# Kernel tuning notes

Hardware: AMD Instinct MI355X
Metric: run time of the kernel (lower is better)

Reference implementation:

```python
import jax, jax.numpy as jnp
import numpy as np

B, S, D, H = 4, 2048, 1024, 16
HD = D // H  # head_dim = 64


def setup_inputs() -> dict:
    key = jax.random.key(0)
    ks = jax.random.split(key, 10)
    sc = 0.02
    return {
        "data": jax.random.normal(ks[0], (B, S, D), jnp.float32),
        "context": jax.random.normal(ks[1], (B, S, D), jnp.float32),
        "Wq": jax.random.normal(ks[2], (D, D), jnp.float32) * sc,
        "bq": jnp.zeros((D,), jnp.float32),
        "Wk": jax.random.normal(ks[3], (D, D), jnp.float32) * sc,
        "bk": jnp.zeros((D,), jnp.float32),
        "Wv": jax.random.normal(ks[4], (D, D), jnp.float32) * sc,
        "bv": jnp.zeros((D,), jnp.float32),
        "Wo": jax.random.normal(ks[5], (D, D), jnp.float32) * sc,
        "bo": jnp.zeros((D,), jnp.float32),
    }


def reference(data, context, Wq, bq, Wk, bk, Wv, bv, Wo, bo):
    # Q/K/V projections (nn.Linear: x @ W^T + b; here weights stored as [in, out])
    Q = data @ Wq + bq            # [B,S,D]
    K = context @ Wk + bk
    V = context @ Wv + bv
    # split heads -> [B,H,S,HD]
    Q = Q.reshape(B, S, H, HD).transpose(0, 2, 1, 3)
    K = K.reshape(B, S, H, HD).transpose(0, 2, 1, 3)
    V = V.reshape(B, S, H, HD).transpose(0, 2, 1, 3)
    scale = jnp.sqrt(jnp.asarray(HD, Q.dtype))
    Z = jnp.einsum("bhqd,bhkd->bhqk", Q, K) / scale   # [B,H,S,S]
    # causal mask: row >= col allowed
    row = jnp.arange(S)[:, None]
    col = jnp.arange(S)[None, :]
    Z = jnp.where(row >= col, Z, jnp.asarray(-jnp.inf, Z.dtype))
    Z = jax.nn.softmax(Z, axis=-1)
    out = jnp.einsum("bhqk,bhkd->bhqd", Z, V)         # [B,H,S,HD]
    out = out.transpose(0, 2, 1, 3).reshape(B, S, D)
    return out @ Wo + bo
```

## Files before the change

### kernel.cpp

```cpp
#include <hip/hip_runtime.h>
#include <hip/hip_bf16.h>

#define B_ 4
#define S_ 2048
#define D_ 1024
#define H_ 16
#define HD_ 64
#define M_ (B_*S_)

typedef __bf16 bf16;
typedef __bf16 bf16v4 __attribute__((ext_vector_type(4)));
typedef __bf16 bf16v8 __attribute__((ext_vector_type(8)));
typedef float f32x4 __attribute__((ext_vector_type(4)));
typedef float f32x16 __attribute__((ext_vector_type(16)));

#define GLDS(gp, lp) __builtin_amdgcn_global_load_lds( \
    (const __attribute__((address_space(1))) void*)(gp), \
    (__attribute__((address_space(3))) void*)(lp), 16, 0, 0)

__global__ void cast_bf16_kernel(const float* __restrict__ in, bf16* __restrict__ out, int n) {
    int i = (blockIdx.x * blockDim.x + threadIdx.x) * 8;
    if (i >= n) return;
    const float4* p = reinterpret_cast<const float4*>(in + i);
    float4 a = p[0], b = p[1];
    bf16v8 o;
    o[0] = (bf16)a.x; o[1] = (bf16)a.y; o[2] = (bf16)a.z; o[3] = (bf16)a.w;
    o[4] = (bf16)b.x; o[5] = (bf16)b.y; o[6] = (bf16)b.z; o[7] = (bf16)b.w;
    *reinterpret_cast<bf16v8*>(out + i) = o;
}

__global__ void transpose_cast_kernel(const float* __restrict__ W, bf16* __restrict__ Wt,
                                      int K, int N, float scale) {
    __shared__ float tile[32][33];
    int kb = blockIdx.y * 32, nb = blockIdx.x * 32;
    int t = threadIdx.x;
    int c = t & 31, r0 = t >> 5;
    for (int i = 0; i < 4; ++i) {
        int r = r0 + i * 8;
        tile[r][c] = W[(size_t)(kb + r) * N + nb + c];
    }
    __syncthreads();
    for (int i = 0; i < 4; ++i) {
        int r = r0 + i * 8;
        Wt[(size_t)(nb + r) * K + kb + c] = (bf16)(tile[c][r] * scale);
    }
}

__global__ void transpose_v_kernel(const bf16* __restrict__ Vb, bf16* __restrict__ Vt) {
    __shared__ bf16 tile[32][33];
    int sb = blockIdx.x * 32;
    int z = blockIdx.y;
    int dt = z & 1, bh = z >> 1;
    int b = bh >> 4, h = bh & 15;
    int t = threadIdx.x;
    int c = t & 31, r0 = t >> 5;
    for (int i = 0; i < 4; ++i) {
        int r = r0 + i * 8;
        tile[r][c] = Vb[(size_t)(b * S_ + sb + r) * D_ + h * HD_ + dt * 32 + c];
    }
    __syncthreads();
    for (int i = 0; i < 4; ++i) {
        int r = r0 + i * 8;
        Vt[((size_t)bh * HD_ + dt * 32 + r) * S_ + sb + c] = tile[c][r];
    }
}

template<bool OUT_F32>
__global__ __launch_bounds__(256) void gemm128_kernel(const bf16* __restrict__ A,
                                                      const bf16* __restrict__ Bt,
                                                      const float* __restrict__ bias,
                                                      float bias_scale,
                                                      void* __restrict__ Cout,
                                                      int M, int N, int K) {
    __shared__ bf16 Asm[128 * 64];
    __shared__ bf16 Bsm[128 * 64];
    int mb = blockIdx.x * 128, nb = blockIdx.y * 128;
    int t = threadIdx.x, l = t & 63, w = t >> 6;
    int wr = w >> 1, wc = w & 1;
    int lg = l >> 4, lr = l & 15;
    f32x4 acc[4][4] = {};
    int srow = t >> 3;
    int schk = t & 7;
    for (int k0 = 0; k0 < K; k0 += 64) {
        __syncthreads();
        #pragma unroll
        for (int p = 0; p < 4; ++p) {
            int row = p * 32 + srow;
            int ca = schk ^ (row & 7);
            GLDS(&A[(size_t)(mb + row) * K + k0 + ca * 8], &Asm[(size_t)(p * 256 + t) * 8]);
            GLDS(&Bt[(size_t)(nb + row) * K + k0 + ca * 8], &Bsm[(size_t)(p * 256 + t) * 8]);
        }
        __syncthreads();
        #pragma unroll
        for (int kk = 0; kk < 2; ++kk) {
            bf16v8 af[4], bfv[4];
            #pragma unroll
            for (int i = 0; i < 4; ++i) {
                int ra = wr * 64 + i * 16 + lr;
                af[i]  = *(const bf16v8*)&Asm[ra * 64 + (((kk * 4 + lg) ^ (ra & 7)) * 8)];
                int rb = wc * 64 + i * 16 + lr;
                bfv[i] = *(const bf16v8*)&Bsm[rb * 64 + (((kk * 4 + lg) ^ (rb & 7)) * 8)];
            }
            #pragma unroll
            for (int i = 0; i < 4; ++i)
                #pragma unroll
                for (int j = 0; j < 4; ++j)
                    acc[i][j] = __builtin_amdgcn_mfma_f32_16x16x32_bf16(af[i], bfv[j], acc[i][j], 0, 0, 0);
        }
    }
    #pragma unroll
    for (int i = 0; i < 4; ++i)
        #pragma unroll
        for (int j = 0; j < 4; ++j) {
            int col = nb + wc * 64 + j * 16 + lr;
            float bv = bias ? bias[col] * bias_scale : 0.f;
            #pragma unroll
            for (int r = 0; r < 4; ++r) {
                int row = mb + wr * 64 + i * 16 + lg * 4 + r;
                float v = acc[i][j][r] + bv;
                if (OUT_F32) ((float*)Cout)[(size_t)row * N + col] = v;
                else         ((bf16*)Cout)[(size_t)row * N + col] = (bf16)v;
            }
        }
}

__global__ __launch_bounds__(256, 2) void attn_kernel(const bf16* __restrict__ Q,
                                                      const bf16* __restrict__ Kb,
                                                      const bf16* __restrict__ Vt,
                                                      bf16* __restrict__ O) {
    __shared__ bf16 Ksm[2][64 * 64];
    __shared__ bf16 Vsm[2][64 * 64];

    int id = (int)blockIdx.x;
    int bh = id & 63;
    int qi = (S_ / 128 - 1) - (id >> 6);
    int qb = qi * 128;
    int b = bh >> 4, h = bh & 15;
    int t = threadIdx.x, w = t >> 6, l = t & 63;
    int ln = l & 31, hi = l >> 5;
    int qwave = qb + w * 32;
    int q = qwave + ln;

    const bf16* kbase = Kb + (size_t)(b * S_) * D_ + h * HD_;
    const bf16* vbase = Vt + (size_t)bh * HD_ * S_;
    const bf16* qptr  = Q + (size_t)(b * S_ + q) * D_ + h * HD_;

    bf16v8 qf[4];
    #pragma unroll
    for (int c = 0; c < 4; ++c)
        qf[c] = *(const bf16v8*)(qptr + c * 16 + hi * 8);

    f32x16 o0 = {}, o1 = {};
    float mrow = -__builtin_inff(), lsum = 0.f;

    int srow = t >> 3, schk = t & 7;
    int nT = 2 * qi + 2;

    auto stage = [&](int kv0, int bufsel) {
        #pragma unroll
        for (int p = 0; p < 2; ++p) {
            int row = p * 32 + srow;
            int cs = schk ^ (row & 7);
            GLDS(kbase + (size_t)(kv0 + row) * D_ + cs * 8, &Ksm[bufsel][p * 2048 + t * 8]);
            GLDS(vbase + (size_t)row * S_ + kv0 + cs * 8,   &Vsm[bufsel][p * 2048 + t * 8]);
        }
    };

    stage(0, 0);
    for (int tt = 0; tt < nT; ++tt) {
        int cur = tt & 1;
        int kv0 = tt * 64;
        __syncthreads();
        if (tt + 1 < nT) stage(kv0 + 64, cur ^ 1);
        if (kv0 > qwave + 31) continue;

        f32x16 st0 = {}, st1 = {};
        __builtin_amdgcn_s_setprio(1);
        #pragma unroll
        for (int c = 0; c < 4; ++c) {
            int r0 = ln;
            bf16v8 kf0 = *(const bf16v8*)&Ksm[cur][r0 * 64 + (((2 * c + hi) ^ (r0 & 7)) * 8)];
            st0 = __builtin_amdgcn_mfma_f32_32x32x16_bf16(kf0, qf[c], st0, 0, 0, 0);
            int r1 = 32 + ln;
            bf16v8 kf1 = *(const bf16v8*)&Ksm[cur][r1 * 64 + (((2 * c + hi) ^ (r1 & 7)) * 8)];
            st1 = __builtin_amdgcn_mfma_f32_32x32x16_bf16(kf1, qf[c], st1, 0, 0, 0);
        }
        __builtin_amdgcn_s_setprio(0);

        if (kv0 + 63 > qwave) {
            #pragma unroll
            for (int rg = 0; rg < 16; ++rg) {
                int kvo = (rg & 3) + 8 * (rg >> 2) + 4 * hi;
                if (kv0 + kvo > q)      st0[rg] = -__builtin_inff();
                if (kv0 + 32 + kvo > q) st1[rg] = -__builtin_inff();
            }
        }

        float tm[16];
        #pragma unroll
        for (int i = 0; i < 16; ++i) tm[i] = fmaxf(st0[i], st1[i]);
        #pragma unroll
        for (int s = 8; s > 0; s >>= 1)
            #pragma unroll
            for (int i = 0; i < s; ++i) tm[i] = fmaxf(tm[i], tm[i + s]);
        float mt = fmaxf(tm[0], __shfl_xor(tm[0], 32, 64));

        if (__any(mt > mrow + 8.f)) {
            float mnew = fmaxf(mrow, mt);
            float sf = __builtin_exp2f(mrow - mnew);
            mrow = mnew;
            lsum *= sf;
            #pragma unroll
            for (int i = 0; i < 16; ++i) { o0[i] *= sf; o1[i] *= sf; }
        }

        #pragma unroll
        for (int i = 0; i < 16; ++i) {
            st0[i] = __builtin_exp2f(st0[i] - mrow);
            st1[i] = __builtin_exp2f(st1[i] - mrow);
        }
        float ts[16];
        #pragma unroll
        for (int i = 0; i < 16; ++i) ts[i] = st0[i] + st1[i];
        #pragma unroll
        for (int s = 8; s > 0; s >>= 1)
            #pragma unroll
            for (int i = 0; i < s; ++i) ts[i] += ts[i + s];
        lsum += ts[0] + __shfl_xor(ts[0], 32, 64);

        uint32_t x0[4][2], x1[4][2];
        #pragma unroll
        for (int j = 0; j < 4; ++j) {
            asm("v_cvt_pk_bf16_f32 %0, %1, %2" : "=v"(x0[j][0]) : "v"(st0[4*j+0]), "v"(st0[4*j+1]));
            asm("v_cvt_pk_bf16_f32 %0, %1, %2" : "=v"(x0[j][1]) : "v"(st0[4*j+2]), "v"(st0[4*j+3]));
            asm("v_cvt_pk_bf16_f32 %0, %1, %2" : "=v"(x1[j][0]) : "v"(st1[4*j+0]), "v"(st1[4*j+1]));
            asm("v_cvt_pk_bf16_f32 %0, %1, %2" : "=v"(x1[j][1]) : "v"(st1[4*j+2]), "v"(st1[4*j+3]));
        }
        union PB { uint32_t u[4]; bf16v8 v; };
        PB pb[4];
        #pragma unroll
        for (int c = 0; c < 4; ++c) {
            uint32_t (*xs)[2] = (c >> 1) ? x1 : x0;
            int cp = c & 1;
            #pragma unroll
            for (int d = 0; d < 2; ++d) {
                uint32_t own_lo = xs[2 * cp][d];
                uint32_t own_hi = xs[2 * cp + 1][d];
                uint32_t par_lo = __shfl_xor(own_lo, 32, 64);
                uint32_t par_hi = __shfl_xor(own_hi, 32, 64);
                pb[c].u[d]     = hi ? par_hi : own_lo;
                pb[c].u[2 + d] = hi ? own_hi : par_lo;
            }
        }

        __builtin_amdgcn_s_setprio(1);
        #pragma unroll
        for (int c = 0; c < 4; ++c) {
            int r0 = ln;
            bf16v8 va0 = *(const bf16v8*)&Vsm[cur][r0 * 64 + (((2 * c + hi) ^ (r0 & 7)) * 8)];
            o0 = __builtin_amdgcn_mfma_f32_32x32x16_bf16(va0, pb[c].v, o0, 0, 0, 0);
            int r1 = 32 + ln;
            bf16v8 va1 = *(const bf16v8*)&Vsm[cur][r1 * 64 + (((2 * c + hi) ^ (r1 & 7)) * 8)];
            o1 = __builtin_amdgcn_mfma_f32_32x32x16_bf16(va1, pb[c].v, o1, 0, 0, 0);
        }
        __builtin_amdgcn_s_setprio(0);
    }

    float li = 1.f / lsum;
    bf16* obase = O + (size_t)(b * S_ + q) * D_ + h * HD_;
    #pragma unroll
    for (int j = 0; j < 4; ++j) {
        bf16v4 ov;
        #pragma unroll
        for (int r = 0; r < 4; ++r) ov[r] = (bf16)(o0[4 * j + r] * li);
        *(bf16v4*)(obase + 8 * j + 4 * hi) = ov;
    }
    #pragma unroll
    for (int j = 0; j < 4; ++j) {
        bf16v4 ov;
        #pragma unroll
        for (int r = 0; r < 4; ++r) ov[r] = (bf16)(o1[4 * j + r] * li);
        *(bf16v4*)(obase + 32 + 8 * j + 4 * hi) = ov;
    }
}

extern "C" void kernel_launch(void* const* d_in, const int* in_sizes, int n_in,
                              void* d_out, int out_size, void* d_ws, size_t ws_size,
                              hipStream_t stream) {
    const float* data    = (const float*)d_in[0];
    const float* context = (const float*)d_in[1];
    const float* Wq = (const float*)d_in[2];
    const float* bq = (const float*)d_in[3];
    const float* Wk = (const float*)d_in[4];
    const float* bk = (const float*)d_in[5];
    const float* Wv = (const float*)d_in[6];
    const float* bv = (const float*)d_in[7];
    const float* Wo = (const float*)d_in[8];
    const float* bo = (const float*)d_in[9];
    float* out = (float*)d_out;

    char* ws = (char*)d_ws;
    size_t off = 0;
    auto alloc = [&](size_t bytes) { void* p = ws + off; off += (bytes + 255) & ~255ull; return p; };
    bf16* dataB = (bf16*)alloc((size_t)M_ * D_ * 2);
    bf16* ctxB  = (bf16*)alloc((size_t)M_ * D_ * 2);
    bf16* WqT   = (bf16*)alloc((size_t)D_ * D_ * 2);
    bf16* WkT   = (bf16*)alloc((size_t)D_ * D_ * 2);
    bf16* WvT   = (bf16*)alloc((size_t)D_ * D_ * 2);
    bf16* WoT   = (bf16*)alloc((size_t)D_ * D_ * 2);
    bf16* Qb    = (bf16*)alloc((size_t)M_ * D_ * 2);
    bf16* Kb    = (bf16*)alloc((size_t)M_ * D_ * 2);
    bf16* Vb    = (bf16*)alloc((size_t)M_ * D_ * 2);
    bf16* Vt    = dataB;
    bf16* Ob    = ctxB;

    const float qscale = 0.125f * 1.44269504088896340736f;

    int nTok = M_ * D_;
    cast_bf16_kernel<<<nTok / 2048, 256, 0, stream>>>(data, dataB, nTok);
    cast_bf16_kernel<<<nTok / 2048, 256, 0, stream>>>(context, ctxB, nTok);

    dim3 tg(D_ / 32, D_ / 32);
    transpose_cast_kernel<<<tg, 256, 0, stream>>>(Wq, WqT, D_, D_, qscale);
    transpose_cast_kernel<<<tg, 256, 0, stream>>>(Wk, WkT, D_, D_, 1.f);
    transpose_cast_kernel<<<tg, 256, 0, stream>>>(Wv, WvT, D_, D_, 1.f);
    transpose_cast_kernel<<<tg, 256, 0, stream>>>(Wo, WoT, D_, D_, 1.f);

    dim3 gg(M_ / 128, D_ / 128);
    gemm128_kernel<false><<<gg, 256, 0, stream>>>(dataB, WqT, bq, qscale, Qb, M_, D_, D_);
    gemm128_kernel<false><<<gg, 256, 0, stream>>>(ctxB,  WkT, bk, 1.f,    Kb, M_, D_, D_);
    gemm128_kernel<false><<<gg, 256, 0, stream>>>(ctxB,  WvT, bv, 1.f,    Vb, M_, D_, D_);

    dim3 vt(S_ / 32, 2 * B_ * H_);
    transpose_v_kernel<<<vt, 256, 0, stream>>>(Vb, Vt);

    attn_kernel<<<dim3(S_ / 128 * B_ * H_), 256, 0, stream>>>(Qb, Kb, Vt, Ob);

    gemm128_kernel<true><<<gg, 256, 0, stream>>>(Ob, WoT, bo, 1.f, out, M_, D_, D_);
}
```

Before: 211.1 us.

## Fuse V transpose into GEMM epilogue, merge prep kernels, widen attention blocks

Merges the two input casts into one launch and the four weight transposes into one launch. The V projection GEMM now writes its output directly in the per-head transposed layout, which removes the separate transpose kernel and its intermediate buffer. The attention kernel moves to 512-thread blocks covering 256 queries, so each staged K/V tile is shared by twice as many query rows. The trade-off is fewer attention blocks, which coarsens causal load balance and may raise register pressure under the new launch bounds.

New measurement: 205.0 us. 2.9% less time.

```diff
diff --git a/kernel.cpp b/kernel.cpp
--- a/kernel.cpp
+++ b/kernel.cpp
@@ -18,54 +18,46 @@
     (const __attribute__((address_space(1))) void*)(gp), \
     (__attribute__((address_space(3))) void*)(lp), 16, 0, 0)
 
-__global__ void cast_bf16_kernel(const float* __restrict__ in, bf16* __restrict__ out, int n) {
-    int i = (blockIdx.x * blockDim.x + threadIdx.x) * 8;
-    if (i >= n) return;
-    const float4* p = reinterpret_cast<const float4*>(in + i);
-    float4 a = p[0], b = p[1];
+__global__ void cast2_bf16_kernel(const float* __restrict__ a, const float* __restrict__ b,
+                                  bf16* __restrict__ oa, bf16* __restrict__ ob, int n) {
+    int gid = blockIdx.x * blockDim.x + threadIdx.x;
+    int i = gid * 8;
+    const float* src; bf16* dst;
+    if (i < n) { src = a + i; dst = oa + i; }
+    else       { src = b + (i - n); dst = ob + (i - n); }
+    const float4* p = reinterpret_cast<const float4*>(src);
+    float4 x = p[0], y = p[1];
     bf16v8 o;
-    o[0] = (bf16)a.x; o[1] = (bf16)a.y; o[2] = (bf16)a.z; o[3] = (bf16)a.w;
-    o[4] = (bf16)b.x; o[5] = (bf16)b.y; o[6] = (bf16)b.z; o[7] = (bf16)b.w;
-    *reinterpret_cast<bf16v8*>(out + i) = o;
-}
-
-__global__ void transpose_cast_kernel(const float* __restrict__ W, bf16* __restrict__ Wt,
-                                      int K, int N, float scale) {
+    o[0] = (bf16)x.x; o[1] = (bf16)x.y; o[2] = (bf16)x.z; o[3] = (bf16)x.w;
+    o[4] = (bf16)y.x; o[5] = (bf16)y.y; o[6] = (bf16)y.z; o[7] = (bf16)y.w;
+    *reinterpret_cast<bf16v8*>(dst) = o;
+}
+
+__global__ void transpose4_kernel(const float* __restrict__ W0, const float* __restrict__ W1,
+                                  const float* __restrict__ W2, const float* __restrict__ W3,
+                                  bf16* __restrict__ T0, bf16* __restrict__ T1,
+                                  bf16* __restrict__ T2, bf16* __restrict__ T3,
+                                  float s0) {
     __shared__ float tile[32][33];
+    int which = blockIdx.z;
+    const float* W = which == 0 ? W0 : which == 1 ? W1 : which == 2 ? W2 : W3;
+    bf16* Wt       = which == 0 ? T0 : which == 1 ? T1 : which == 2 ? T2 : T3;
+    float scale    = which == 0 ? s0 : 1.f;
     int kb = blockIdx.y * 32, nb = blockIdx.x * 32;
     int t = threadIdx.x;
     int c = t & 31, r0 = t >> 5;
     for (int i = 0; i < 4; ++i) {
         int r = r0 + i * 8;
-        tile[r][c] = W[(size_t)(kb + r) * N + nb + c];
+        tile[r][c] = W[(size_t)(kb + r) * D_ + nb + c];
     }
     __syncthreads();
     for (int i = 0; i < 4; ++i) {
         int r = r0 + i * 8;
-        Wt[(size_t)(nb + r) * K + kb + c] = (bf16)(tile[c][r] * scale);
-    }
-}
-
-__global__ void transpose_v_kernel(const bf16* __restrict__ Vb, bf16* __restrict__ Vt) {
-    __shared__ bf16 tile[32][33];
-    int sb = blockIdx.x * 32;
-    int z = blockIdx.y;
-    int dt = z & 1, bh = z >> 1;
-    int b = bh >> 4, h = bh & 15;
-    int t = threadIdx.x;
-    int c = t & 31, r0 = t >> 5;
-    for (int i = 0; i < 4; ++i) {
-        int r = r0 + i * 8;
-        tile[r][c] = Vb[(size_t)(b * S_ + sb + r) * D_ + h * HD_ + dt * 32 + c];
-    }
-    __syncthreads();
-    for (int i = 0; i < 4; ++i) {
-        int r = r0 + i * 8;
-        Vt[((size_t)bh * HD_ + dt * 32 + r) * S_ + sb + c] = tile[c][r];
-    }
-}
-
-template<bool OUT_F32>
+        Wt[(size_t)(nb + r) * D_ + kb + c] = (bf16)(tile[c][r] * scale);
+    }
+}
+
+template<int MODE>
 __global__ __launch_bounds__(256) void gemm128_kernel(const bf16* __restrict__ A,
                                                       const bf16* __restrict__ Bt,
                                                       const float* __restrict__ bias,
@@ -114,17 +106,27 @@
         for (int j = 0; j < 4; ++j) {
             int col = nb + wc * 64 + j * 16 + lr;
             float bv = bias ? bias[col] * bias_scale : 0.f;
-            #pragma unroll
-            for (int r = 0; r < 4; ++r) {
-                int row = mb + wr * 64 + i * 16 + lg * 4 + r;
-                float v = acc[i][j][r] + bv;
-                if (OUT_F32) ((float*)Cout)[(size_t)row * N + col] = v;
-                else         ((bf16*)Cout)[(size_t)row * N + col] = (bf16)v;
+            int row0 = mb + wr * 64 + i * 16 + lg * 4;
+            if (MODE == 2) {
+                int b = row0 >> 11, s = row0 & 2047;
+                int bh = b * 16 + (col >> 6), hd = col & 63;
+                bf16v4 ov;
+                #pragma unroll
+                for (int r = 0; r < 4; ++r) ov[r] = (bf16)(acc[i][j][r] + bv);
+                *(bf16v4*)&((bf16*)Cout)[((size_t)bh * 64 + hd) * 2048 + s] = ov;
+            } else {
+                #pragma unroll
+                for (int r = 0; r < 4; ++r) {
+                    int row = row0 + r;
+                    float v = acc[i][j][r] + bv;
+                    if (MODE == 1) ((float*)Cout)[(size_t)row * N + col] = v;
+                    else           ((bf16*)Cout)[(size_t)row * N + col] = (bf16)v;
+                }
             }
         }
 }
 
-__global__ __launch_bounds__(256, 2) void attn_kernel(const bf16* __restrict__ Q,
+__global__ __launch_bounds__(512, 4) void attn_kernel(const bf16* __restrict__ Q,
                                                       const bf16* __restrict__ Kb,
                                                       const bf16* __restrict__ Vt,
                                                       bf16* __restrict__ O) {
@@ -133,8 +135,8 @@
 
     int id = (int)blockIdx.x;
     int bh = id & 63;
-    int qi = (S_ / 128 - 1) - (id >> 6);
-    int qb = qi * 128;
+    int qi = (S_ / 256 - 1) - (id >> 6);
+    int qb = qi * 256;
     int b = bh >> 4, h = bh & 15;
     int t = threadIdx.x, w = t >> 6, l = t & 63;
     int ln = l & 31, hi = l >> 5;
@@ -154,16 +156,12 @@
     float mrow = -__builtin_inff(), lsum = 0.f;
 
     int srow = t >> 3, schk = t & 7;
-    int nT = 2 * qi + 2;
+    int nT = 4 * qi + 4;
 
     auto stage = [&](int kv0, int bufsel) {
-        #pragma unroll
-        for (int p = 0; p < 2; ++p) {
-            int row = p * 32 + srow;
-            int cs = schk ^ (row & 7);
-            GLDS(kbase + (size_t)(kv0 + row) * D_ + cs * 8, &Ksm[bufsel][p * 2048 + t * 8]);
-            GLDS(vbase + (size_t)row * S_ + kv0 + cs * 8,   &Vsm[bufsel][p * 2048 + t * 8]);
-        }
+        int cs = schk ^ (srow & 7);
+        GLDS(kbase + (size_t)(kv0 + srow) * D_ + cs * 8, &Ksm[bufsel][t * 8]);
+        GLDS(vbase + (size_t)srow * S_ + kv0 + cs * 8,   &Vsm[bufsel][t * 8]);
     };
 
     stage(0, 0);
@@ -310,31 +308,23 @@
     bf16* WoT   = (bf16*)alloc((size_t)D_ * D_ * 2);
     bf16* Qb    = (bf16*)alloc((size_t)M_ * D_ * 2);
     bf16* Kb    = (bf16*)alloc((size_t)M_ * D_ * 2);
-    bf16* Vb    = (bf16*)alloc((size_t)M_ * D_ * 2);
-    bf16* Vt    = dataB;
+    bf16* Vt    = (bf16*)alloc((size_t)M_ * D_ * 2);
     bf16* Ob    = ctxB;
 
     const float qscale = 0.125f * 1.44269504088896340736f;
 
     int nTok = M_ * D_;
-    cast_bf16_kernel<<<nTok / 2048, 256, 0, stream>>>(data, dataB, nTok);
-    cast_bf16_kernel<<<nTok / 2048, 256, 0, stream>>>(context, ctxB, nTok);
-
-    dim3 tg(D_ / 32, D_ / 32);
-    transpose_cast_kernel<<<tg, 256, 0, stream>>>(Wq, WqT, D_, D_, qscale);
-    transpose_cast_kernel<<<tg, 256, 0, stream>>>(Wk, WkT, D_, D_, 1.f);
-    transpose_cast_kernel<<<tg, 256, 0, stream>>>(Wv, WvT, D_, D_, 1.f);
-    transpose_cast_kernel<<<tg, 256, 0, stream>>>(Wo, WoT, D_, D_, 1.f);
+    cast2_bf16_kernel<<<2 * nTok / 2048, 256, 0, stream>>>(data, context, dataB, ctxB, nTok);
+
+    dim3 tg(D_ / 32, D_ / 32, 4);
+    transpose4_kernel<<<tg, 256, 0, stream>>>(Wq, Wk, Wv, Wo, WqT, WkT, WvT, WoT, qscale);
 
     dim3 gg(M_ / 128, D_ / 128);
-    gemm128_kernel<false><<<gg, 256, 0, stream>>>(dataB, WqT, bq, qscale, Qb, M_, D_, D_);
-    gemm128_kernel<false><<<gg, 256, 0, stream>>>(ctxB,  WkT, bk, 1.f,    Kb, M_, D_, D_);
-    gemm128_kernel<false><<<gg, 256, 0, stream>>>(ctxB,  WvT, bv, 1.f,    Vb, M_, D_, D_);
-
-    dim3 vt(S_ / 32, 2 * B_ * H_);
-    transpose_v_kernel<<<vt, 256, 0, stream>>>(Vb, Vt);
-
-    attn_kernel<<<dim3(S_ / 128 * B_ * H_), 256, 0, stream>>>(Qb, Kb, Vt, Ob);
-
-    gemm128_kernel<true><<<gg, 256, 0, stream>>>(Ob, WoT, bo, 1.f, out, M_, D_, D_);
-}
+    gemm128_kernel<0><<<gg, 256, 0, stream>>>(dataB, WqT, bq, qscale, Qb, M_, D_, D_);
+    gemm128_kernel<0><<<gg, 256, 0, stream>>>(ctxB,  WkT, bk, 1.f,    Kb, M_, D_, D_);
+    gemm128_kernel<2><<<gg, 256, 0, stream>>>(ctxB,  WvT, bv, 1.f,    Vt, M_, D_, D_);
+
+    attn_kernel<<<dim3(S_ / 256 * B_ * H_), 512, 0, stream>>>(Qb, Kb, Vt, Ob);
+
+    gemm128_kernel<1><<<gg, 256, 0, stream>>>(Ob, WoT, bo, 1.f, out, M_, D_, D_);
+}
```
